# Kernel tuning notes

Hardware: AMD Instinct MI355X
Metric: run time of the kernel (lower is better)

Reference implementation:

```python
import jax, jax.numpy as jnp
import numpy as np

B, S, D, H, FD = 2, 2048, 1024, 16, 64
DK = D // H
ALPHA = 1.0


def _l2norm(t):
    # matches F.normalize(p=2, dim=-1): divide by max(norm, eps)
    n = jnp.linalg.norm(t, axis=-1, keepdims=True)
    return t / jnp.maximum(n, 1e-12)


def setup_inputs() -> dict:
    key = jax.random.key(0)
    ks = jax.random.split(key, 12)
    sc = 0.02
    return {
        "x": jax.random.normal(ks[0], (B, S, D), jnp.float32),
        "features": jax.random.normal(ks[1], (B, S, FD), jnp.float32),
        "requirements": jax.random.normal(ks[2], (B, S, FD), jnp.float32),
        "Wq": jax.random.normal(ks[3], (D, D), jnp.float32) * sc,
        "bq": jnp.zeros((D,), jnp.float32),
        "Wk": jax.random.normal(ks[4], (D, D), jnp.float32) * sc,
        "bk": jnp.zeros((D,), jnp.float32),
        "Wv": jax.random.normal(ks[5], (D, D), jnp.float32) * sc,
        "bv": jnp.zeros((D,), jnp.float32),
        "Wo": jax.random.normal(ks[6], (D, D), jnp.float32) * sc,
        "bo": jnp.zeros((D,), jnp.float32),
        "pos_ids": jax.random.randint(ks[7], (B, S), 0, 8),
        "causal_mask": jnp.tril(jnp.ones((S, S), bool)),
    }


def reference(x, features, requirements, Wq, bq, Wk, bk, Wv, bv, Wo, bo,
              pos_ids, causal_mask):
    # q/k/v projections -> [B, S, H, DK]
    Q = (x @ Wq + bq).reshape(B, S, H, DK)
    K = (x @ Wk + bk).reshape(B, S, H, DK)
    V = (x @ Wv + bv).reshape(B, S, H, DK)

    # scaled QK^T: [B, H, S, S]
    scores = jnp.einsum('bshd,bthd->bhst', Q, K) / np.sqrt(DK).astype(np.float32)

    # ASA bias (features_only mode): cosine compat req_i . feat_j -> [B, S, S]
    bias = jnp.einsum('bsf,btf->bst', _l2norm(requirements), _l2norm(features))
    scores = scores + ALPHA * bias[:, None, :, :]

    # causal mask (True = allowed)
    scores = jnp.where(causal_mask[None, None, :, :], scores, -jnp.inf)

    weights = jax.nn.softmax(scores, axis=-1)
    weights = jnp.nan_to_num(weights, nan=0.0)

    out = jnp.einsum('bhst,bthd->bshd', weights, V).reshape(B, S, D)
    return out @ Wo + bo
```

## Files before the change

### kernel.cpp

```cpp
#include <hip/hip_runtime.h>
#include <hip/hip_bf16.h>
#include <math.h>

#define Bb 2
#define Ss 2048
#define Dd 1024
#define Hh 16
#define DK 64
#define FD 64

#define LOG2E 1.4426950408889634f

typedef short short8 __attribute__((ext_vector_type(8)));
typedef float f32x4 __attribute__((ext_vector_type(4)));
typedef unsigned int u32;

static __device__ inline ushort f2bf(float f) {
    union { float f; unsigned u; } v; v.f = f;
    unsigned r = v.u + 0x7FFF + ((v.u >> 16) & 1);
    return (ushort)(r >> 16);
}

static __device__ inline uint cvt_pk_bf16(float lo, float hi) {
    uint r;
    asm("v_cvt_pk_bf16_f32 %0, %1, %2" : "=v"(r) : "v"(lo), "v"(hi));
    return r;
}
static __device__ inline float fexp2(float x) {
    return __builtin_amdgcn_exp2f(x);
}

static __device__ inline void gload_lds16(const ushort* g, ushort* l) {
    __builtin_amdgcn_global_load_lds((const __attribute__((address_space(1))) u32*)g,
                                     (__attribute__((address_space(3))) u32*)l, 16, 0, 0);
}

__global__ __launch_bounds__(256) void prep(const float* __restrict__ x,
                                            const float* __restrict__ features,
                                            const float* __restrict__ requirements,
                                            const float* __restrict__ W0,
                                            const float* __restrict__ W1,
                                            const float* __restrict__ W2,
                                            const float* __restrict__ W3,
                                            ushort* __restrict__ WT,
                                            ushort* __restrict__ xb,
                                            ushort* __restrict__ Qext,
                                            ushort* __restrict__ Kext) {
    __shared__ float T[64][65];
    const int blk = blockIdx.x;
    const int tid = threadIdx.x;

    if (blk < 8192) {
        size_t p = (size_t)blk * 256 + tid;
        float2 v = *(const float2*)(x + 2 * p);
        ((uint*)xb)[p] = (uint)f2bf(v.x) | ((uint)f2bf(v.y) << 16);
        return;
    }
    if (blk < 9216) {
        const int f = blk - 8192;
        const int bx = f & 15, by = (f >> 4) & 15, bz = f >> 8;
        const float* W = bz == 0 ? W0 : bz == 1 ? W1 : bz == 2 ? W2 : W3;
        ushort* dst = WT + (size_t)bz * Dd * Dd;
        const int k0 = bx * 64, n0 = by * 64;
#pragma unroll
        for (int i = 0; i < 4; ++i) {
            int kr = i * 16 + (tid >> 4);
            int nc = (tid & 15) * 4;
            float4 v = *(const float4*)(W + (size_t)(k0 + kr) * Dd + n0 + nc);
            T[kr][nc] = v.x; T[kr][nc + 1] = v.y; T[kr][nc + 2] = v.z; T[kr][nc + 3] = v.w;
        }
        __syncthreads();
        int nr = tid >> 2;
        int kc = (tid & 3) * 16;
        uint pk[8];
#pragma unroll
        for (int j = 0; j < 8; ++j)
            pk[j] = (uint)f2bf(T[kc + 2 * j][nr]) | ((uint)f2bf(T[kc + 2 * j + 1][nr]) << 16);
        uint* o = (uint*)(dst + (size_t)(n0 + nr) * Dd + k0 + kc);
        *(int4*)o = *(int4*)&pk[0];
        *(int4*)(o + 4) = *(int4*)&pk[4];
        return;
    }
    {
        const int f3 = blk - 9216;
        const int row = f3 * 4 + (tid >> 6);
        const int lane = tid & 63;
        const int b = row >> 11, s = row & (Ss - 1);
        const int j = lane & 31;
        const float* src = (lane < 32) ? features : requirements;
        float2 v = *(const float2*)(src + (size_t)row * FD + 2 * j);
        float ss = v.x * v.x + v.y * v.y;
#pragma unroll
        for (int off = 16; off; off >>= 1) ss += __shfl_xor(ss, off, 64);
        const float inv = 1.0f / fmaxf(sqrtf(ss), 1e-12f);
        const float scl = (lane < 32) ? inv : inv * LOG2E;
        const uint pk = cvt_pk_bf16(v.x * scl, v.y * scl);
        uint* dstq = (uint*)Qext;
        uint* dstk = (uint*)Kext;
#pragma unroll
        for (int h = 0; h < 16; ++h) {
            size_t rowq = ((size_t)(b * Hh + h) * Ss + s) * 64 + 32 + j;
            if (lane < 32) dstk[rowq] = pk;
            else           dstq[rowq] = pk;
        }
    }
}

__global__ __launch_bounds__(256) void gemm_qkv(const ushort* __restrict__ xb,
                                                const ushort* __restrict__ WT,
                                                const float* __restrict__ bq,
                                                const float* __restrict__ bk,
                                                const float* __restrict__ bv,
                                                ushort* __restrict__ Qext,
                                                ushort* __restrict__ Kext,
                                                ushort* __restrict__ Vt) {
    __shared__ ushort smem[17408];
    ushort (*As)[64] = (ushort (*)[64])smem;
    ushort (*Bs)[64] = (ushort (*)[64])(smem + 8192);
    const int tid = threadIdx.x;
    const int lane = tid & 63, wave = tid >> 6;
    const int col = lane & 15, quad = lane >> 4;
    const int wm = wave >> 1, wn = wave & 1;
    const int flat = blockIdx.x + 24 * blockIdx.y;
    const int xcd = flat & 7;
    const int jj = flat >> 3;
    const int id = jj % 3;
    const int n0 = xcd * 128;
    const int m0 = (jj / 3) * 128;
    const ushort* BTw = WT + (size_t)id * Dd * Dd;
    const float* bias = id == 0 ? bq : id == 1 ? bk : bv;

    const int l8 = lane >> 3;
    const int srcg = (lane & 7) ^ l8;
    const ushort* aS[4]; const ushort* bS[4];
    ushort* aD[4]; ushort* bD[4];
#pragma unroll
    for (int i = 0; i < 4; ++i) {
        int r = wave * 32 + i * 8 + l8;
        aS[i] = xb  + (size_t)(m0 + r) * Dd + srcg * 8;
        bS[i] = BTw + (size_t)(n0 + r) * Dd + srcg * 8;
        aD[i] = smem + (wave * 4 + i) * 512;
        bD[i] = smem + 8192 + (wave * 4 + i) * 512;
    }
    const int xs = col & 7;

    f32x4 acc[4][4] = {};

    for (int k0 = 0; k0 < Dd; k0 += 64) {
        __syncthreads();
#pragma unroll
        for (int i = 0; i < 4; ++i) {
            gload_lds16(aS[i] + k0, aD[i]);
            gload_lds16(bS[i] + k0, bD[i]);
        }
        __syncthreads();
#pragma unroll
        for (int kk = 0; kk < 2; ++kk) {
            short8 af[4], bf[4];
#pragma unroll
            for (int i = 0; i < 4; ++i) {
                af[i] = *(const short8*)&As[wm * 64 + i * 16 + col][((kk * 4 + quad) ^ xs) * 8];
                bf[i] = *(const short8*)&Bs[wn * 64 + i * 16 + col][((kk * 4 + quad) ^ xs) * 8];
            }
#pragma unroll
            for (int i = 0; i < 4; ++i)
#pragma unroll
                for (int j = 0; j < 4; ++j)
                    acc[i][j] = __builtin_amdgcn_mfma_f32_16x16x32_bf16(af[i], bf[j], acc[i][j], 0, 0, 0);
        }
    }

    __syncthreads();
    ushort (*Ep)[136] = (ushort (*)[136])smem;
    const float scl = (id == 0) ? 0.125f * LOG2E : 1.0f;
#pragma unroll
    for (int j = 0; j < 4; ++j) {
        int n_local = wn * 64 + j * 16 + col;
        float bvl = bias[n0 + n_local];
#pragma unroll
        for (int i = 0; i < 4; ++i) {
            int mb = wm * 64 + i * 16 + quad * 4;
#pragma unroll
            for (int reg = 0; reg < 4; ++reg)
                Ep[mb + reg][n_local] = f2bf((acc[i][j][reg] + bvl) * scl);
        }
    }
    __syncthreads();
    if (id == 2) {
        const int b = m0 >> 11, s0 = m0 & (Ss - 1);
#pragma unroll
        for (int it = 0; it < 32; ++it) {
            int n_local = wave * 32 + it;
            int hh = (n0 >> 6) + (n_local >> 6);
            int d = n_local & 63;
            uint pk = (uint)Ep[lane * 2][n_local] | ((uint)Ep[lane * 2 + 1][n_local] << 16);
            uint* dst = (uint*)(Vt + ((size_t)((b * Hh + hh) * DK + d)) * Ss + s0);
            dst[lane] = pk;
        }
    } else {
        const int mrow = tid >> 1;
        const int half = tid & 1;
        const int b = m0 >> 11, s = (m0 & (Ss - 1)) + mrow;
        const int hh = (n0 >> 6) + half;
        ushort* drow = (id == 0 ? Qext : Kext) + ((size_t)(b * Hh + hh) * Ss + s) * 128;
#pragma unroll
        for (int k = 0; k < 8; ++k)
            *(int4*)(drow + k * 8) = *(int4*)&Ep[mrow][half * 64 + k * 8];
    }
}

__global__ __launch_bounds__(256) void gemm_out(const ushort* __restrict__ Ab,
                                                const ushort* __restrict__ BT,
                                                const float* __restrict__ bias,
                                                float* __restrict__ C) {
    __shared__ ushort As[128][64];
    __shared__ ushort Bs[128][64];
    const int tid = threadIdx.x;
    const int lane = tid & 63, wave = tid >> 6;
    const int col = lane & 15, quad = lane >> 4;
    const int wm = wave >> 1, wn = wave & 1;
    const int n0 = blockIdx.x * 128;
    const int m0 = blockIdx.y * 128;

    const int l8 = lane >> 3;
    const int srcg = (lane & 7) ^ l8;
    const ushort* aS[4]; const ushort* bS[4];
    ushort* aD[4]; ushort* bD[4];
#pragma unroll
    for (int i = 0; i < 4; ++i) {
        int r = wave * 32 + i * 8 + l8;
        aS[i] = Ab + (size_t)(m0 + r) * Dd + srcg * 8;
        bS[i] = BT + (size_t)(n0 + r) * Dd + srcg * 8;
        aD[i] = &As[0][0] + (wave * 4 + i) * 512;
        bD[i] = &Bs[0][0] + (wave * 4 + i) * 512;
    }
    const int xs = col & 7;

    f32x4 acc[4][4] = {};

    for (int k0 = 0; k0 < Dd; k0 += 64) {
        __syncthreads();
#pragma unroll
        for (int i = 0; i < 4; ++i) {
            gload_lds16(aS[i] + k0, aD[i]);
            gload_lds16(bS[i] + k0, bD[i]);
        }
        __syncthreads();
#pragma unroll
        for (int kk = 0; kk < 2; ++kk) {
            short8 af[4], bf[4];
#pragma unroll
            for (int i = 0; i < 4; ++i) {
                af[i] = *(const short8*)&As[wm * 64 + i * 16 + col][((kk * 4 + quad) ^ xs) * 8];
                bf[i] = *(const short8*)&Bs[wn * 64 + i * 16 + col][((kk * 4 + quad) ^ xs) * 8];
            }
#pragma unroll
            for (int i = 0; i < 4; ++i)
#pragma unroll
                for (int j = 0; j < 4; ++j)
                    acc[i][j] = __builtin_amdgcn_mfma_f32_16x16x32_bf16(af[i], bf[j], acc[i][j], 0, 0, 0);
        }
    }

#pragma unroll
    for (int j = 0; j < 4; ++j) {
        int n = n0 + wn * 64 + j * 16 + col;
        float bvl = bias[n];
#pragma unroll
        for (int i = 0; i < 4; ++i) {
#pragma unroll
            for (int reg = 0; reg < 4; ++reg) {
                int m = m0 + wm * 64 + i * 16 + quad * 4 + reg;
                C[(size_t)m * Dd + n] = acc[i][j][reg] + bvl;
            }
        }
    }
}

#define ABQ 128

__global__ __launch_bounds__(512) void attn_mfma14(const ushort* __restrict__ Qe,
                                                   const ushort* __restrict__ Ke,
                                                   const ushort* __restrict__ Vt,
                                                   ushort* __restrict__ Ob) {
    __shared__ ushort Ks[64][128];
    __shared__ ushort Vts[64][64];
    __shared__ ushort PsT[8][16][64];

    const int tid = threadIdx.x;
    const int wave = tid >> 6, lane = tid & 63;
    const int col = lane & 15, quad = lane >> 4;

    const int id = blockIdx.x;
    const int x = id & 7;
    const int k = id >> 3;
    const int rep = k & 1;
    const int bhi = (k >> 1) & 3;
    const int qh = k >> 3;
    const int bh = bhi * 8 + x;
    const int qt = rep ? (qh < 4 ? qh + 4 : 15 - qh)
                       : (qh < 4 ? qh : 19 - qh);
    const int b = bh >> 4, h = bh & 15;
    const int q0 = qt * ABQ;
    const int rowb = q0 + wave * 16;

    short8 qf[4];
    {
        const ushort* qp = Qe + ((size_t)bh * Ss + rowb + col) * 128 + quad * 8;
#pragma unroll
        for (int k0 = 0; k0 < 4; ++k0) qf[k0] = *(const short8*)(qp + k0 * 32);
    }

    const f32x4 zero4 = {0.f, 0.f, 0.f, 0.f};
    f32x4 oaccT[4] = {zero4, zero4, zero4, zero4};
    float lsum = 0.f;

    const ushort* Kbase = Ke + (size_t)bh * Ss * 128;
    const ushort* Vbase = Vt + (size_t)bh * 64 * Ss;
    const int xsw = col & 7;

    const int Gk0 = wave * 64 + lane;
    const int rk0 = Gk0 >> 4, sk0 = (Gk0 & 15) ^ (rk0 & 7);
    const int Gk1 = 512 + Gk0;
    const int rk1 = Gk1 >> 4, sk1 = (Gk1 & 15) ^ (rk1 & 7);
    const int Gv = Gk0;
    const int rv = Gv >> 3, sv = (Gv & 7) ^ (rv & 7);
    const ushort* ksrc0 = Kbase + (size_t)rk0 * 128 + sk0 * 8;
    const ushort* ksrc1 = Kbase + (size_t)rk1 * 128 + sk1 * 8;
    const ushort* vsrc  = Vbase + (size_t)rv * Ss + sv * 8;
    ushort* kdst0 = &Ks[0][0] + wave * 512;
    ushort* kdst1 = &Ks[0][0] + 4096 + wave * 512;
    ushort* vdst  = &Vts[0][0] + wave * 512;

    const int ntiles = 2 * qt + 2;
    for (int t = 0; t < ntiles; ++t) {
        const int j0 = t * 64;
        __syncthreads();
        gload_lds16(ksrc0, kdst0);   ksrc0 += 64 * 128;
        gload_lds16(ksrc1, kdst1);   ksrc1 += 64 * 128;
        gload_lds16(vsrc,  vdst);    vsrc  += 64;
        __syncthreads();

        if (j0 > rowb + 15) continue;

        f32x4 sacc[4] = {zero4, zero4, zero4, zero4};
        __builtin_amdgcn_s_setprio(1);
#pragma unroll
        for (int c = 0; c < 4; ++c)
#pragma unroll
            for (int k0 = 0; k0 < 4; ++k0) {
                short8 kf = *(const short8*)&Ks[c * 16 + col][((k0 * 4 + quad) ^ xsw) * 8];
                sacc[c] = __builtin_amdgcn_mfma_f32_16x16x32_bf16(kf, qf[k0], sacc[c], 0, 0, 0);
            }
        __builtin_amdgcn_s_setprio(0);

        const bool diag = (j0 + 63 >= rowb);
        if (diag) {
            const int qrow_rel = rowb + col - j0;
#pragma unroll
            for (int c = 0; c < 4; ++c)
#pragma unroll
                for (int reg = 0; reg < 4; ++reg) {
                    float s = sacc[c][reg];
                    if (c * 16 + quad * 4 + reg > qrow_rel) s = -1e9f;
                    float p = fexp2(fminf(s, 28.853901f));
                    lsum += p;
                    sacc[c][reg] = p;
                }
        } else {
#pragma unroll
            for (int c = 0; c < 4; ++c)
#pragma unroll
                for (int reg = 0; reg < 4; ++reg) {
                    float p = fexp2(fminf(sacc[c][reg], 28.853901f));
                    lsum += p;
                    sacc[c][reg] = p;
                }
        }
#pragma unroll
        for (int c = 0; c < 4; ++c) {
            uint2 pk;
            pk.x = cvt_pk_bf16(sacc[c][0], sacc[c][1]);
            pk.y = cvt_pk_bf16(sacc[c][2], sacc[c][3]);
            *(uint2*)&PsT[wave][col][((c * 2 + (quad >> 1)) ^ xsw) * 8 + (quad & 1) * 4] = pk;
        }

        __builtin_amdgcn_s_setprio(1);
#pragma unroll
        for (int k0 = 0; k0 < 2; ++k0) {
            short8 ptf = *(const short8*)&PsT[wave][col][((k0 * 4 + quad) ^ xsw) * 8];
#pragma unroll
            for (int c2 = 0; c2 < 4; ++c2) {
                short8 vtf = *(const short8*)&Vts[c2 * 16 + col][((k0 * 4 + quad) ^ xsw) * 8];
                oaccT[c2] = __builtin_amdgcn_mfma_f32_16x16x32_bf16(vtf, ptf, oaccT[c2], 0, 0, 0);
            }
        }
        __builtin_amdgcn_s_setprio(0);
    }

    {
        float l = lsum;
        l += __shfl_xor(l, 16, 64);
        l += __shfl_xor(l, 32, 64);
        const float inv = 1.f / l;
        ushort* dst = Ob + ((size_t)b * Ss + rowb + col) * Dd + h * DK + quad * 4;
#pragma unroll
        for (int c2 = 0; c2 < 4; ++c2) {
            uint2 pk;
            pk.x = cvt_pk_bf16(oaccT[c2][0] * inv, oaccT[c2][1] * inv);
            pk.y = cvt_pk_bf16(oaccT[c2][2] * inv, oaccT[c2][3] * inv);
            *(uint2*)(dst + c2 * 16) = pk;
        }
    }
}

extern "C" void kernel_launch(void* const* d_in, const int* in_sizes, int n_in,
                              void* d_out, int out_size, void* d_ws, size_t ws_size,
                              hipStream_t stream) {
    const float* x            = (const float*)d_in[0];
    const float* features     = (const float*)d_in[1];
    const float* requirements = (const float*)d_in[2];
    const float* Wq = (const float*)d_in[3];
    const float* bq = (const float*)d_in[4];
    const float* Wk = (const float*)d_in[5];
    const float* bk = (const float*)d_in[6];
    const float* Wv = (const float*)d_in[7];
    const float* bv = (const float*)d_in[8];
    const float* Wo = (const float*)d_in[9];
    const float* bo = (const float*)d_in[10];

    float* out = (float*)d_out;
    float* ws = (float*)d_ws;

    ushort* xb   = (ushort*)(ws);
    ushort* WT   = (ushort*)(ws + 2097152);
    ushort* Qext = (ushort*)(ws + 4194304);
    ushort* Kext = (ushort*)(ws + 8388608);
    ushort* Vt   = (ushort*)(ws + 16777216);
    ushort* abb  = (ushort*)(ws + 12582912);

    prep<<<10240, 256, 0, stream>>>(x, features, requirements, Wq, Wk, Wv, Wo,
                                    WT, xb, Qext, Kext);

    gemm_qkv<<<dim3(24, 32), 256, 0, stream>>>(xb, WT, bq, bk, bv, Qext, Kext, Vt);

    attn_mfma14<<<dim3(512), 512, 0, stream>>>(Qext, Kext, Vt, abb);

    gemm_out<<<dim3(8, 32), 256, 0, stream>>>(abb, WT + (size_t)3 * Dd * Dd, bo, out);
}
```

Baseline: 225.6 us.

## Store normalized bias features once per batch instead of replicating per head

The prep kernel no longer writes the normalized features/requirements into all 16 per-head extended Q/K rows. It stores them once per batch row in compact buffers. The QKV GEMM now writes 64-wide Q/K instead of 128-wide. The attention kernel assembles the extended Q fragments and K tiles from the separate head-specific and shared buffers. This removes redundant global writes and shrinks the workspace. In exchange, the K tile loads use a per-lane pointer select and the data-layout invariants become more intricate.

```diff
diff --git a/kernel.cpp b/kernel.cpp
--- a/kernel.cpp
+++ b/kernel.cpp
@@ -44,8 +44,8 @@
                                             const float* __restrict__ W3,
                                             ushort* __restrict__ WT,
                                             ushort* __restrict__ xb,
-                                            ushort* __restrict__ Qext,
-                                            ushort* __restrict__ Kext) {
+                                            ushort* __restrict__ fnc,
+                                            ushort* __restrict__ rnc) {
     __shared__ float T[64][65];
     const int blk = blockIdx.x;
     const int tid = threadIdx.x;
@@ -85,7 +85,6 @@
         const int f3 = blk - 9216;
         const int row = f3 * 4 + (tid >> 6);
         const int lane = tid & 63;
-        const int b = row >> 11, s = row & (Ss - 1);
         const int j = lane & 31;
         const float* src = (lane < 32) ? features : requirements;
         float2 v = *(const float2*)(src + (size_t)row * FD + 2 * j);
@@ -95,14 +94,8 @@
         const float inv = 1.0f / fmaxf(sqrtf(ss), 1e-12f);
         const float scl = (lane < 32) ? inv : inv * LOG2E;
         const uint pk = cvt_pk_bf16(v.x * scl, v.y * scl);
-        uint* dstq = (uint*)Qext;
-        uint* dstk = (uint*)Kext;
-#pragma unroll
-        for (int h = 0; h < 16; ++h) {
-            size_t rowq = ((size_t)(b * Hh + h) * Ss + s) * 64 + 32 + j;
-            if (lane < 32) dstk[rowq] = pk;
-            else           dstq[rowq] = pk;
-        }
+        if (lane < 32) ((uint*)fnc)[(size_t)row * 32 + j] = pk;
+        else           ((uint*)rnc)[(size_t)row * 32 + j] = pk;
     }
 }
 
@@ -111,8 +104,8 @@
                                                 const float* __restrict__ bq,
                                                 const float* __restrict__ bk,
                                                 const float* __restrict__ bv,
-                                                ushort* __restrict__ Qext,
-                                                ushort* __restrict__ Kext,
+                                                ushort* __restrict__ Qm,
+                                                ushort* __restrict__ Km,
                                                 ushort* __restrict__ Vt) {
     __shared__ ushort smem[17408];
     ushort (*As)[64] = (ushort (*)[64])smem;
@@ -202,7 +195,7 @@
         const int half = tid & 1;
         const int b = m0 >> 11, s = (m0 & (Ss - 1)) + mrow;
         const int hh = (n0 >> 6) + half;
-        ushort* drow = (id == 0 ? Qext : Kext) + ((size_t)(b * Hh + hh) * Ss + s) * 128;
+        ushort* drow = (id == 0 ? Qm : Km) + ((size_t)(b * Hh + hh) * Ss + s) * 64;
 #pragma unroll
         for (int k = 0; k < 8; ++k)
             *(int4*)(drow + k * 8) = *(int4*)&Ep[mrow][half * 64 + k * 8];
@@ -279,8 +272,10 @@
 
 #define ABQ 128
 
-__global__ __launch_bounds__(512) void attn_mfma14(const ushort* __restrict__ Qe,
-                                                   const ushort* __restrict__ Ke,
+__global__ __launch_bounds__(512) void attn_mfma16(const ushort* __restrict__ Qm,
+                                                   const ushort* __restrict__ Km,
+                                                   const ushort* __restrict__ fnc,
+                                                   const ushort* __restrict__ rnc,
                                                    const ushort* __restrict__ Vt,
                                                    ushort* __restrict__ Ob) {
     __shared__ ushort Ks[64][128];
@@ -306,16 +301,20 @@
 
     short8 qf[4];
     {
-        const ushort* qp = Qe + ((size_t)bh * Ss + rowb + col) * 128 + quad * 8;
-#pragma unroll
-        for (int k0 = 0; k0 < 4; ++k0) qf[k0] = *(const short8*)(qp + k0 * 32);
+        const ushort* qpm = Qm + ((size_t)bh * Ss + rowb + col) * 64 + quad * 8;
+        const ushort* qpa = rnc + ((size_t)(b * Ss) + rowb + col) * 64 + quad * 8;
+        qf[0] = *(const short8*)qpm;
+        qf[1] = *(const short8*)(qpm + 32);
+        qf[2] = *(const short8*)qpa;
+        qf[3] = *(const short8*)(qpa + 32);
     }
 
     const f32x4 zero4 = {0.f, 0.f, 0.f, 0.f};
     f32x4 oaccT[4] = {zero4, zero4, zero4, zero4};
     float lsum = 0.f;
 
-    const ushort* Kbase = Ke + (size_t)bh * Ss * 128;
+    const ushort* Kbase = Km + (size_t)bh * Ss * 64;
+    const ushort* Abase = fnc + (size_t)b * Ss * 64;
     const ushort* Vbase = Vt + (size_t)bh * 64 * Ss;
     const int xsw = col & 7;
 
@@ -325,8 +324,10 @@
     const int rk1 = Gk1 >> 4, sk1 = (Gk1 & 15) ^ (rk1 & 7);
     const int Gv = Gk0;
     const int rv = Gv >> 3, sv = (Gv & 7) ^ (rv & 7);
-    const ushort* ksrc0 = Kbase + (size_t)rk0 * 128 + sk0 * 8;
-    const ushort* ksrc1 = Kbase + (size_t)rk1 * 128 + sk1 * 8;
+    const ushort* ksrc0 = (sk0 < 8 ? Kbase + (size_t)rk0 * 64 + sk0 * 8
+                                   : Abase + (size_t)rk0 * 64 + (sk0 - 8) * 8);
+    const ushort* ksrc1 = (sk1 < 8 ? Kbase + (size_t)rk1 * 64 + sk1 * 8
+                                   : Abase + (size_t)rk1 * 64 + (sk1 - 8) * 8);
     const ushort* vsrc  = Vbase + (size_t)rv * Ss + sv * 8;
     ushort* kdst0 = &Ks[0][0] + wave * 512;
     ushort* kdst1 = &Ks[0][0] + 4096 + wave * 512;
@@ -336,8 +337,8 @@
     for (int t = 0; t < ntiles; ++t) {
         const int j0 = t * 64;
         __syncthreads();
-        gload_lds16(ksrc0, kdst0);   ksrc0 += 64 * 128;
-        gload_lds16(ksrc1, kdst1);   ksrc1 += 64 * 128;
+        gload_lds16(ksrc0, kdst0);   ksrc0 += 64 * 64;
+        gload_lds16(ksrc1, kdst1);   ksrc1 += 64 * 64;
         gload_lds16(vsrc,  vdst);    vsrc  += 64;
         __syncthreads();
 
@@ -434,17 +435,19 @@
 
     ushort* xb   = (ushort*)(ws);
     ushort* WT   = (ushort*)(ws + 2097152);
-    ushort* Qext = (ushort*)(ws + 4194304);
-    ushort* Kext = (ushort*)(ws + 8388608);
-    ushort* Vt   = (ushort*)(ws + 16777216);
-    ushort* abb  = (ushort*)(ws + 12582912);
+    ushort* Qm   = (ushort*)(ws + 4194304);
+    ushort* Km   = (ushort*)(ws + 6291456);
+    ushort* Vt   = (ushort*)(ws + 8388608);
+    ushort* abb  = (ushort*)(ws + 10485760);
+    ushort* fnc  = (ushort*)(ws + 12582912);
+    ushort* rnc  = (ushort*)(ws + 12713984);
 
     prep<<<10240, 256, 0, stream>>>(x, features, requirements, Wq, Wk, Wv, Wo,
-                                    WT, xb, Qext, Kext);
-
-    gemm_qkv<<<dim3(24, 32), 256, 0, stream>>>(xb, WT, bq, bk, bv, Qext, Kext, Vt);
-
-    attn_mfma14<<<dim3(512), 512, 0, stream>>>(Qext, Kext, Vt, abb);
+                                    WT, xb, fnc, rnc);
+
+    gemm_qkv<<<dim3(24, 32), 256, 0, stream>>>(xb, WT, bq, bk, bv, Qm, Km, Vt);
+
+    attn_mfma16<<<dim3(512), 512, 0, stream>>>(Qm, Km, fnc, rnc, Vt, abb);
 
     gemm_out<<<dim3(8, 32), 256, 0, stream>>>(abb, WT + (size_t)3 * Dd * Dd, bo, out);
 }
```

Measured after the change: 223.8 us. Within noise of the previous version (-0.8%).
